# Optimization experiments

Hardware: AMD Instinct MI355X
Metric: run time of the kernel (lower is better)

Reference implementation:

```python
import jax, jax.numpy as jnp
import numpy as np

B, S, H, I, E, TOPK = 2, 2048, 1024, 2048, 8, 2


def setup_inputs() -> dict:
    key = jax.random.key(0)
    k0, k1, k2, k3, k4 = jax.random.split(key, 5)
    return {
        "hidden_state": jax.random.normal(k0, (B, S, H), dtype=jnp.float32),
        "gate_w": jax.random.normal(k1, (H, E), dtype=jnp.float32) * 0.02,
        "Wg": jax.random.normal(k2, (E, H, I), dtype=jnp.float32) * 0.02,
        "Wu": jax.random.normal(k3, (E, H, I), dtype=jnp.float32) * 0.02,
        "Wd": jax.random.normal(k4, (E, I, H), dtype=jnp.float32) * 0.02,
        "top_k": TOPK,
    }


def reference(hidden_state, gate_w, Wg, Wu, Wd, top_k):
    b, s, h = hidden_state.shape
    x = hidden_state.reshape(-1, h)                      # [T, H]
    T = x.shape[0]
    router_logits = x @ gate_w                           # [T, E]
    probs = jax.nn.softmax(router_logits, axis=-1)
    top_p, top_i = jax.lax.top_k(probs, top_k)           # [T, K]
    # norm_expert=False -> no renormalization of top-k probs
    # scatter top-k probs into dense per-expert combine weights [T, E]
    weights = jnp.zeros((T, probs.shape[-1]), dtype=x.dtype)
    weights = weights.at[jnp.arange(T)[:, None], top_i].add(top_p)
    # dense per-expert SwiGLU MLP (equivalent math to gather/scatter dispatch)
    g = jnp.einsum('th,ehi->tei', x, Wg)                 # [T, E, I]
    u = jnp.einsum('th,ehi->tei', x, Wu)
    mid = jax.nn.silu(g) * u
    expert_out = jnp.einsum('tei,eih->teh', mid, Wd)     # [T, E, H]
    final = jnp.einsum('te,teh->th', weights, expert_out)
    return final.reshape(b, s, h), router_logits
```

## Files before the change

kernel.cpp:

```cpp
#include <hip/hip_runtime.h>
#include <stdint.h>
#include <math.h>

#define T_TOK 4096
#define H_DIM 1024
#define I_DIM 2048
#define E_NUM 8
#define PMAX (T_TOK * 2 + E_NUM * 128)

typedef __attribute__((ext_vector_type(8))) short short8;
typedef __attribute__((ext_vector_type(4))) float f32x4;
typedef unsigned short u16;
typedef unsigned int u32;

__device__ __forceinline__ u16 f2bf(float f) {
  union { float f; u32 u; } v; v.f = f;
  u32 r = v.u + 0x7fffu + ((v.u >> 16) & 1u);
  return (u16)(r >> 16);
}
__device__ __forceinline__ float bf2f(u16 a) {
  union { u32 u; float f; } v; v.u = ((u32)a) << 16; return v.f;
}

__device__ __forceinline__ void async_ld16(const u16* g, u16* l) {
  __builtin_amdgcn_global_load_lds(
      (const __attribute__((address_space(1))) void*)g,
      (__attribute__((address_space(3))) void*)l, 16, 0, 0);
}

__global__ void prep_kernel(const float* __restrict__ x, u16* __restrict__ xb,
                            const float* __restrict__ gw, float* __restrict__ gwT, int n4) {
  int i = blockIdx.x * blockDim.x + threadIdx.x;
  int stride = gridDim.x * blockDim.x;
  for (int j = i; j < n4; j += stride) {
    float4 v = ((const float4*)x)[j];
    ushort4 o;
    o.x = f2bf(v.x); o.y = f2bf(v.y); o.z = f2bf(v.z); o.w = f2bf(v.w);
    ((ushort4*)xb)[j] = o;
  }
  if (i < H_DIM * E_NUM) {
    int r = i >> 3, e = i & 7;
    gwT[e * H_DIM + r] = gw[i];
  }
}

__global__ void wconv_kernel(const float* __restrict__ Wg, const float* __restrict__ Wu,
                             const float* __restrict__ Wd, u16* __restrict__ wgt,
                             u16* __restrict__ wut, u16* __restrict__ wdt) {
  const int zz = blockIdx.z;
  const float* src = (zz == 0) ? Wg : (zz == 1) ? Wu : Wd;
  u16* dst = (zz == 0) ? wgt : (zz == 1) ? wut : wdt;
  const int R = (zz == 2) ? I_DIM : H_DIM;
  const int C = (zz == 2) ? H_DIM : I_DIM;
  const int cpt = C >> 6;
  const int e = blockIdx.x >> 9;
  const int ti = blockIdx.x & 511;
  const int r0 = (ti / cpt) << 6;
  const int c0 = (ti % cpt) << 6;
  const float* s = src + (size_t)e * H_DIM * I_DIM;
  u16* d = dst + (size_t)e * H_DIM * I_DIM;

  const int wave = threadIdx.x >> 6, lane = threadIdx.x & 63;
  const int g = lane >> 4, lq = lane & 15;
  const int c = c0 + wave * 16 + g * 4;
  const int r = r0 + lq * 4;

  float4 v0 = *(const float4*)(s + (size_t)(r + 0) * C + c);
  float4 v1 = *(const float4*)(s + (size_t)(r + 1) * C + c);
  float4 v2 = *(const float4*)(s + (size_t)(r + 2) * C + c);
  float4 v3 = *(const float4*)(s + (size_t)(r + 3) * C + c);

  ushort4 o;
  o.x = f2bf(v0.x); o.y = f2bf(v1.x); o.z = f2bf(v2.x); o.w = f2bf(v3.x);
  *(ushort4*)(d + (size_t)(c + 0) * R + r) = o;
  o.x = f2bf(v0.y); o.y = f2bf(v1.y); o.z = f2bf(v2.y); o.w = f2bf(v3.y);
  *(ushort4*)(d + (size_t)(c + 1) * R + r) = o;
  o.x = f2bf(v0.z); o.y = f2bf(v1.z); o.z = f2bf(v2.z); o.w = f2bf(v3.z);
  *(ushort4*)(d + (size_t)(c + 2) * R + r) = o;
  o.x = f2bf(v0.w); o.y = f2bf(v1.w); o.z = f2bf(v2.w); o.w = f2bf(v3.w);
  *(ushort4*)(d + (size_t)(c + 3) * R + r) = o;
}

__global__ void router_kernel(const float* __restrict__ x, const float* __restrict__ gwT,
                              float* __restrict__ logits_out, int* __restrict__ te,
                              float* __restrict__ tw) {
  const int wave = threadIdx.x >> 6, lane = threadIdx.x & 63;
  const int t = blockIdx.x * 4 + wave;
  const float* xr = x + (size_t)t * H_DIM;
  float acc[8];
#pragma unroll
  for (int e = 0; e < 8; e++) acc[e] = 0.f;
#pragma unroll
  for (int it = 0; it < 4; it++) {
    int h0 = it * 256 + lane * 4;
    float4 xv = *(const float4*)(xr + h0);
#pragma unroll
    for (int e = 0; e < 8; e++) {
      float4 g = *(const float4*)(gwT + e * H_DIM + h0);
      acc[e] += xv.x * g.x + xv.y * g.y + xv.z * g.z + xv.w * g.w;
    }
  }
#pragma unroll
  for (int m = 1; m < 64; m <<= 1) {
#pragma unroll
    for (int e = 0; e < 8; e++) acc[e] += __shfl_xor(acc[e], m, 64);
  }
  if (lane == 0) {
    float mx = acc[0];
#pragma unroll
    for (int e = 1; e < 8; e++) mx = fmaxf(mx, acc[e]);
    float p[8]; float s = 0.f;
#pragma unroll
    for (int e = 0; e < 8; e++) { p[e] = __expf(acc[e] - mx); s += p[e]; }
    float inv = 1.0f / s;
    int e0 = 0; float b0 = acc[0];
#pragma unroll
    for (int e = 1; e < 8; e++) if (acc[e] > b0) { b0 = acc[e]; e0 = e; }
    int e1 = -1; float b1 = -1e30f;
#pragma unroll
    for (int e = 0; e < 8; e++) if (e != e0 && acc[e] > b1) { b1 = acc[e]; e1 = e; }
#pragma unroll
    for (int e = 0; e < 8; e++) logits_out[(size_t)t * 8 + e] = acc[e];
    te[t * 2] = e0; te[t * 2 + 1] = e1;
    tw[t * 2] = p[e0] * inv; tw[t * 2 + 1] = p[e1] * inv;
  }
}

__global__ __launch_bounds__(1024) void sort_kernel(const int* __restrict__ te,
                                                    int* __restrict__ offs,
                                                    int* __restrict__ token_list,
                                                    int* __restrict__ tpos) {
  __shared__ int wsum[16][8];
  __shared__ int wbase[16][8];
  __shared__ int soffs[9];
  const int tid = threadIdx.x;
  const int wave = tid >> 6, lane = tid & 63;

  for (int j = tid; j < PMAX; j += 1024) token_list[j] = 0;

  const int t0 = tid * 4;
  int e_loc[8];
  int cnt[8];
#pragma unroll
  for (int e = 0; e < 8; e++) cnt[e] = 0;
#pragma unroll
  for (int k = 0; k < 8; k++) {
    int e = te[t0 * 2 + k];
    e_loc[k] = e;
    cnt[e]++;
  }
  int excl[8];
#pragma unroll
  for (int e = 0; e < 8; e++) {
    int v = cnt[e];
    int s = v;
#pragma unroll
    for (int d = 1; d < 64; d <<= 1) {
      int u = __shfl_up(s, d, 64);
      if (lane >= d) s += u;
    }
    excl[e] = s - v;
    if (lane == 63) wsum[wave][e] = s;
  }
  __syncthreads();
  if (tid < 8) {
    int e = tid;
    int a = 0;
    for (int w2 = 0; w2 < 16; w2++) { wbase[w2][e] = a; a += wsum[w2][e]; }
    wsum[0][e] = a;
  }
  __syncthreads();
  if (tid == 0) {
    int a = 0;
    for (int e = 0; e < 8; e++) {
      soffs[e] = a;
      a += (wsum[0][e] + 127) & ~127;
    }
    soffs[8] = a;
    for (int e = 0; e <= 8; e++) offs[e] = soffs[e];
  }
  __syncthreads();
  int base[8];
#pragma unroll
  for (int e = 0; e < 8; e++) base[e] = soffs[e] + wbase[wave][e] + excl[e];
#pragma unroll
  for (int k = 0; k < 8; k++) {
    int e = e_loc[k];
    int pos = base[e]++;
    int t = t0 + (k >> 1);
    token_list[pos] = t;
    tpos[t * 2 + (k & 1)] = pos;
  }
}

#define BK1 64

__global__ __launch_bounds__(256, 2) void gemm1_kernel(
    const u16* __restrict__ xb, const u16* __restrict__ wgt, const u16* __restrict__ wut,
    const int* __restrict__ token_list, const int* __restrict__ offs, u16* __restrict__ mid) {
  const int e = blockIdx.z;
  const int off = offs[e];
  const int pcount = offs[e + 1] - off;
  const int row0 = blockIdx.y * 128;
  if (row0 >= pcount) return;
  const int n0 = blockIdx.x * 128;

  __shared__ __align__(16) u16 As[128 * BK1];
  __shared__ __align__(16) u16 Bg[128 * BK1];
  __shared__ __align__(16) u16 Bu[128 * BK1];

  const int tid = threadIdx.x;
  const int wave = tid >> 6, lane = tid & 63;
  const int wm = (wave >> 1) * 64, wn = (wave & 1) * 64;
  const int quad = lane >> 4, lr = lane & 15;
  const int l7 = lr & 7;

  f32x4 accg[4][4], accu[4][4];
  f32x4 z = {0.f, 0.f, 0.f, 0.f};
#pragma unroll
  for (int i = 0; i < 4; i++)
#pragma unroll
    for (int j = 0; j < 4; j++) { accg[i][j] = z; accu[i][j] = z; }

  const u16* wgb = wgt + (size_t)e * I_DIM * H_DIM;
  const u16* wub = wut + (size_t)e * I_DIM * H_DIM;

  const u16* ga[4]; const u16* gg[4]; const u16* gu[4];
  u16 *la[4], *lg[4], *lu[4];
#pragma unroll
  for (int i = 0; i < 4; i++) {
    int c = tid + 256 * i;
    int row = c >> 3, kcl = c & 7;
    int kg = kcl ^ (row & 7);
    int tok = token_list[off + row0 + row];
    ga[i] = xb + (size_t)tok * H_DIM + kg * 8;
    gg[i] = wgb + (size_t)(n0 + row) * H_DIM + kg * 8;
    gu[i] = wub + (size_t)(n0 + row) * H_DIM + kg * 8;
    la[i] = &As[c * 8]; lg[i] = &Bg[c * 8]; lu[i] = &Bu[c * 8];
  }

  for (int kt = 0; kt < H_DIM / BK1; kt++) {
    const int k0 = kt * BK1;
#pragma unroll
    for (int i = 0; i < 4; i++) {
      async_ld16(ga[i] + k0, la[i]);
      async_ld16(gg[i] + k0, lg[i]);
      async_ld16(gu[i] + k0, lu[i]);
    }
    __syncthreads();
#pragma unroll
    for (int kk = 0; kk < 2; kk++) {
      const int slot = ((kk << 2) + quad) ^ l7;
      short8 af[4];
#pragma unroll
      for (int im = 0; im < 4; im++)
        af[im] = *(const short8*)(&As[(wm + im * 16 + lr) * BK1 + slot * 8]);
#pragma unroll
      for (int in = 0; in < 4; in++) {
        short8 bg = *(const short8*)(&Bg[(wn + in * 16 + lr) * BK1 + slot * 8]);
        short8 bu = *(const short8*)(&Bu[(wn + in * 16 + lr) * BK1 + slot * 8]);
#pragma unroll
        for (int im = 0; im < 4; im++) {
          accg[im][in] = __builtin_amdgcn_mfma_f32_16x16x32_bf16(af[im], bg, accg[im][in], 0, 0, 0);
          accu[im][in] = __builtin_amdgcn_mfma_f32_16x16x32_bf16(af[im], bu, accu[im][in], 0, 0, 0);
        }
      }
    }
    __syncthreads();
  }

#pragma unroll
  for (int im = 0; im < 4; im++) {
#pragma unroll
    for (int r = 0; r < 4; r++) {
      int row = row0 + wm + im * 16 + quad * 4 + r;
      u16* mrow = mid + (size_t)(off + row) * I_DIM + n0 + wn;
#pragma unroll
      for (int in = 0; in < 4; in++) {
        float g = accg[im][in][r];
        float u = accu[im][in][r];
        float sv = g / (1.0f + __expf(-g)) * u;
        mrow[in * 16 + lr] = f2bf(sv);
      }
    }
  }
}

__global__ __launch_bounds__(256, 2) void gemm2_kernel(
    const u16* __restrict__ mid, const u16* __restrict__ wdt,
    const int* __restrict__ offs, u16* __restrict__ eout) {
  const int e = blockIdx.z;
  const int off = offs[e];
  const int pcount = offs[e + 1] - off;
  const int row0 = blockIdx.y * 128;
  if (row0 >= pcount) return;
  const int n0 = blockIdx.x * 128;

  __shared__ __align__(16) u16 As[128 * BK1];
  __shared__ __align__(16) u16 Bs[128 * BK1];

  const int tid = threadIdx.x;
  const int wave = tid >> 6, lane = tid & 63;
  const int wm = (wave >> 1) * 64, wn = (wave & 1) * 64;
  const int quad = lane >> 4, lr = lane & 15;
  const int l7 = lr & 7;

  f32x4 acc[4][4];
  f32x4 z = {0.f, 0.f, 0.f, 0.f};
#pragma unroll
  for (int i = 0; i < 4; i++)
#pragma unroll
    for (int j = 0; j < 4; j++) acc[i][j] = z;

  const u16* wdb = wdt + (size_t)e * H_DIM * I_DIM;

  const u16* ga[4]; const u16* gb[4];
  u16 *la[4], *lb[4];
#pragma unroll
  for (int i = 0; i < 4; i++) {
    int c = tid + 256 * i;
    int row = c >> 3, kcl = c & 7;
    int kg = kcl ^ (row & 7);
    ga[i] = mid + (size_t)(off + row0 + row) * I_DIM + kg * 8;
    gb[i] = wdb + (size_t)(n0 + row) * I_DIM + kg * 8;
    la[i] = &As[c * 8]; lb[i] = &Bs[c * 8];
  }

  for (int kt = 0; kt < I_DIM / BK1; kt++) {
    const int k0 = kt * BK1;
#pragma unroll
    for (int i = 0; i < 4; i++) {
      async_ld16(ga[i] + k0, la[i]);
      async_ld16(gb[i] + k0, lb[i]);
    }
    __syncthreads();
#pragma unroll
    for (int kk = 0; kk < 2; kk++) {
      const int slot = ((kk << 2) + quad) ^ l7;
      short8 af[4];
#pragma unroll
      for (int im = 0; im < 4; im++)
        af[im] = *(const short8*)(&As[(wm + im * 16 + lr) * BK1 + slot * 8]);
#pragma unroll
      for (int in = 0; in < 4; in++) {
        short8 bf = *(const short8*)(&Bs[(wn + in * 16 + lr) * BK1 + slot * 8]);
#pragma unroll
        for (int im = 0; im < 4; im++)
          acc[im][in] = __builtin_amdgcn_mfma_f32_16x16x32_bf16(af[im], bf, acc[im][in], 0, 0, 0);
      }
    }
    __syncthreads();
  }

#pragma unroll
  for (int im = 0; im < 4; im++) {
#pragma unroll
    for (int r = 0; r < 4; r++) {
      int row = row0 + wm + im * 16 + quad * 4 + r;
      u16* orow = eout + (size_t)(off + row) * H_DIM + n0 + wn;
#pragma unroll
      for (int in = 0; in < 4; in++)
        orow[in * 16 + lr] = f2bf(acc[im][in][r]);
    }
  }
}

__global__ void combine_kernel(const u16* __restrict__ eout, const int* __restrict__ tpos,
                               const float* __restrict__ tw, float* __restrict__ out) {
  const int half = threadIdx.x >> 7;
  const int t = blockIdx.x * 2 + half;
  const int lt = threadIdx.x & 127;
  const int h0 = lt * 8;
  const int p0 = tpos[t * 2], p1 = tpos[t * 2 + 1];
  const float w0 = tw[t * 2], w1 = tw[t * 2 + 1];
  ushort4 a0 = *(const ushort4*)(eout + (size_t)p0 * H_DIM + h0);
  ushort4 a1 = *(const ushort4*)(eout + (size_t)p0 * H_DIM + h0 + 4);
  ushort4 b0 = *(const ushort4*)(eout + (size_t)p1 * H_DIM + h0);
  ushort4 b1 = *(const ushort4*)(eout + (size_t)p1 * H_DIM + h0 + 4);
  float4 o0, o1;
  o0.x = w0 * bf2f(a0.x) + w1 * bf2f(b0.x);
  o0.y = w0 * bf2f(a0.y) + w1 * bf2f(b0.y);
  o0.z = w0 * bf2f(a0.z) + w1 * bf2f(b0.z);
  o0.w = w0 * bf2f(a0.w) + w1 * bf2f(b0.w);
  o1.x = w0 * bf2f(a1.x) + w1 * bf2f(b1.x);
  o1.y = w0 * bf2f(a1.y) + w1 * bf2f(b1.y);
  o1.z = w0 * bf2f(a1.z) + w1 * bf2f(b1.z);
  o1.w = w0 * bf2f(a1.w) + w1 * bf2f(b1.w);
  float* orow = out + (size_t)t * H_DIM + h0;
  *(float4*)(orow) = o0;
  *(float4*)(orow + 4) = o1;
}

extern "C" void kernel_launch(void* const* d_in, const int* in_sizes, int n_in,
                              void* d_out, int out_size, void* d_ws, size_t ws_size,
                              hipStream_t stream) {
  const float* x  = (const float*)d_in[0];
  const float* gw = (const float*)d_in[1];
  const float* Wg = (const float*)d_in[2];
  const float* Wu = (const float*)d_in[3];
  const float* Wd = (const float*)d_in[4];
  float* out = (float*)d_out;
  float* out_logits = out + (size_t)T_TOK * H_DIM;

  char* w = (char*)d_ws;
  size_t o = 0;
  auto take = [&](size_t bytes) { char* p = w + o; o += (bytes + 255) & ~(size_t)255; return p; };
  int*   offs        = (int*)take((E_NUM + 1) * 4);
  int*   te          = (int*)take((size_t)T_TOK * 2 * 4);
  float* tw          = (float*)take((size_t)T_TOK * 2 * 4);
  int*   token_list  = (int*)take((size_t)PMAX * 4);
  int*   tpos        = (int*)take((size_t)T_TOK * 2 * 4);
  float* gwT         = (float*)take((size_t)E_NUM * H_DIM * 4);
  u16*   xb          = (u16*)take((size_t)T_TOK * H_DIM * 2);
  u16*   wgt         = (u16*)take((size_t)E_NUM * H_DIM * I_DIM * 2);
  u16*   wut         = (u16*)take((size_t)E_NUM * H_DIM * I_DIM * 2);
  u16*   wdt         = (u16*)take((size_t)E_NUM * H_DIM * I_DIM * 2);
  u16*   mid         = (u16*)take((size_t)PMAX * I_DIM * 2);
  u16*   eout        = wgt;
  (void)in_sizes; (void)n_in; (void)out_size; (void)ws_size;

  prep_kernel<<<512, 256, 0, stream>>>(x, xb, gw, gwT, T_TOK * H_DIM / 4);
  wconv_kernel<<<dim3(E_NUM * 512, 1, 3), 256, 0, stream>>>(Wg, Wu, Wd, wgt, wut, wdt);
  router_kernel<<<T_TOK / 4, 256, 0, stream>>>(x, gwT, out_logits, te, tw);
  sort_kernel<<<1, 1024, 0, stream>>>(te, offs, token_list, tpos);
  gemm1_kernel<<<dim3(I_DIM / 128, PMAX / 128, E_NUM), 256, 0, stream>>>(xb, wgt, wut, token_list, offs, mid);
  gemm2_kernel<<<dim3(H_DIM / 128, PMAX / 128, E_NUM), 256, 0, stream>>>(mid, wdt, offs, eout);
  combine_kernel<<<T_TOK / 2, 256, 0, stream>>>(eout, tpos, tw, out);
}
```

Measured before the change: 420.1 us.

## Fuse weight conversion, x cast and router into one front kernel; raise GEMM occupancy hints

Merges the weight bf16 transpose, activation bf16 cast and router into a single launch. Router blocks stage the transposed gate weights in shared memory, which removes the separate gwT buffer and pass. Launch bounds on the two grouped GEMMs are raised to request more resident blocks per CU. Risks are register spills in the GEMMs and the 32KB static LDS lowering occupancy of the weight-conversion blocks.

```diff
diff --git a/kernel.cpp b/kernel.cpp
--- a/kernel.cpp
+++ b/kernel.cpp
@@ -8,6 +8,9 @@
 #define E_NUM 8
 #define PMAX (T_TOK * 2 + E_NUM * 128)
 
+#define WCONV_BLOCKS (E_NUM * 512 * 3)
+#define ROUTER_BLOCKS (T_TOK / 4)
+
 typedef __attribute__((ext_vector_type(8))) short short8;
 typedef __attribute__((ext_vector_type(4))) float f32x4;
 typedef unsigned short u16;
@@ -28,101 +31,103 @@
       (__attribute__((address_space(3))) void*)l, 16, 0, 0);
 }
 
-__global__ void prep_kernel(const float* __restrict__ x, u16* __restrict__ xb,
-                            const float* __restrict__ gw, float* __restrict__ gwT, int n4) {
-  int i = blockIdx.x * blockDim.x + threadIdx.x;
-  int stride = gridDim.x * blockDim.x;
-  for (int j = i; j < n4; j += stride) {
-    float4 v = ((const float4*)x)[j];
+__global__ void front_kernel(const float* __restrict__ Wg, const float* __restrict__ Wu,
+                             const float* __restrict__ Wd, u16* __restrict__ wgt,
+                             u16* __restrict__ wut, u16* __restrict__ wdt,
+                             const float* __restrict__ x, u16* __restrict__ xb,
+                             const float* __restrict__ gw, float* __restrict__ logits_out,
+                             int* __restrict__ te, float* __restrict__ tw) {
+  __shared__ float sgw[E_NUM * H_DIM];
+  const int b = blockIdx.x;
+  if (b < WCONV_BLOCKS) {
+    const int zz = b / (E_NUM * 512);
+    const int idx = b - zz * (E_NUM * 512);
+    const float* src = (zz == 0) ? Wg : (zz == 1) ? Wu : Wd;
+    u16* dst = (zz == 0) ? wgt : (zz == 1) ? wut : wdt;
+    const int R = (zz == 2) ? I_DIM : H_DIM;
+    const int C = (zz == 2) ? H_DIM : I_DIM;
+    const int cpt = C >> 6;
+    const int e = idx >> 9;
+    const int ti = idx & 511;
+    const int r0 = (ti / cpt) << 6;
+    const int c0 = (ti % cpt) << 6;
+    const float* s = src + (size_t)e * H_DIM * I_DIM;
+    u16* d = dst + (size_t)e * H_DIM * I_DIM;
+
+    const int wave = threadIdx.x >> 6, lane = threadIdx.x & 63;
+    const int g = lane >> 4, lq = lane & 15;
+    const int c = c0 + wave * 16 + g * 4;
+    const int r = r0 + lq * 4;
+
+    float4 v0 = *(const float4*)(s + (size_t)(r + 0) * C + c);
+    float4 v1 = *(const float4*)(s + (size_t)(r + 1) * C + c);
+    float4 v2 = *(const float4*)(s + (size_t)(r + 2) * C + c);
+    float4 v3 = *(const float4*)(s + (size_t)(r + 3) * C + c);
+
     ushort4 o;
-    o.x = f2bf(v.x); o.y = f2bf(v.y); o.z = f2bf(v.z); o.w = f2bf(v.w);
-    ((ushort4*)xb)[j] = o;
-  }
-  if (i < H_DIM * E_NUM) {
-    int r = i >> 3, e = i & 7;
-    gwT[e * H_DIM + r] = gw[i];
-  }
-}
-
-__global__ void wconv_kernel(const float* __restrict__ Wg, const float* __restrict__ Wu,
-                             const float* __restrict__ Wd, u16* __restrict__ wgt,
-                             u16* __restrict__ wut, u16* __restrict__ wdt) {
-  const int zz = blockIdx.z;
-  const float* src = (zz == 0) ? Wg : (zz == 1) ? Wu : Wd;
-  u16* dst = (zz == 0) ? wgt : (zz == 1) ? wut : wdt;
-  const int R = (zz == 2) ? I_DIM : H_DIM;
-  const int C = (zz == 2) ? H_DIM : I_DIM;
-  const int cpt = C >> 6;
-  const int e = blockIdx.x >> 9;
-  const int ti = blockIdx.x & 511;
-  const int r0 = (ti / cpt) << 6;
-  const int c0 = (ti % cpt) << 6;
-  const float* s = src + (size_t)e * H_DIM * I_DIM;
-  u16* d = dst + (size_t)e * H_DIM * I_DIM;
-
-  const int wave = threadIdx.x >> 6, lane = threadIdx.x & 63;
-  const int g = lane >> 4, lq = lane & 15;
-  const int c = c0 + wave * 16 + g * 4;
-  const int r = r0 + lq * 4;
-
-  float4 v0 = *(const float4*)(s + (size_t)(r + 0) * C + c);
-  float4 v1 = *(const float4*)(s + (size_t)(r + 1) * C + c);
-  float4 v2 = *(const float4*)(s + (size_t)(r + 2) * C + c);
-  float4 v3 = *(const float4*)(s + (size_t)(r + 3) * C + c);
-
-  ushort4 o;
-  o.x = f2bf(v0.x); o.y = f2bf(v1.x); o.z = f2bf(v2.x); o.w = f2bf(v3.x);
-  *(ushort4*)(d + (size_t)(c + 0) * R + r) = o;
-  o.x = f2bf(v0.y); o.y = f2bf(v1.y); o.z = f2bf(v2.y); o.w = f2bf(v3.y);
-  *(ushort4*)(d + (size_t)(c + 1) * R + r) = o;
-  o.x = f2bf(v0.z); o.y = f2bf(v1.z); o.z = f2bf(v2.z); o.w = f2bf(v3.z);
-  *(ushort4*)(d + (size_t)(c + 2) * R + r) = o;
-  o.x = f2bf(v0.w); o.y = f2bf(v1.w); o.z = f2bf(v2.w); o.w = f2bf(v3.w);
-  *(ushort4*)(d + (size_t)(c + 3) * R + r) = o;
-}
-
-__global__ void router_kernel(const float* __restrict__ x, const float* __restrict__ gwT,
-                              float* __restrict__ logits_out, int* __restrict__ te,
-                              float* __restrict__ tw) {
-  const int wave = threadIdx.x >> 6, lane = threadIdx.x & 63;
-  const int t = blockIdx.x * 4 + wave;
-  const float* xr = x + (size_t)t * H_DIM;
-  float acc[8];
-#pragma unroll
-  for (int e = 0; e < 8; e++) acc[e] = 0.f;
-#pragma unroll
-  for (int it = 0; it < 4; it++) {
-    int h0 = it * 256 + lane * 4;
-    float4 xv = *(const float4*)(xr + h0);
-#pragma unroll
-    for (int e = 0; e < 8; e++) {
-      float4 g = *(const float4*)(gwT + e * H_DIM + h0);
-      acc[e] += xv.x * g.x + xv.y * g.y + xv.z * g.z + xv.w * g.w;
-    }
-  }
-#pragma unroll
-  for (int m = 1; m < 64; m <<= 1) {
-#pragma unroll
-    for (int e = 0; e < 8; e++) acc[e] += __shfl_xor(acc[e], m, 64);
-  }
-  if (lane == 0) {
-    float mx = acc[0];
-#pragma unroll
-    for (int e = 1; e < 8; e++) mx = fmaxf(mx, acc[e]);
-    float p[8]; float s = 0.f;
-#pragma unroll
-    for (int e = 0; e < 8; e++) { p[e] = __expf(acc[e] - mx); s += p[e]; }
-    float inv = 1.0f / s;
-    int e0 = 0; float b0 = acc[0];
-#pragma unroll
-    for (int e = 1; e < 8; e++) if (acc[e] > b0) { b0 = acc[e]; e0 = e; }
-    int e1 = -1; float b1 = -1e30f;
-#pragma unroll
-    for (int e = 0; e < 8; e++) if (e != e0 && acc[e] > b1) { b1 = acc[e]; e1 = e; }
-#pragma unroll
-    for (int e = 0; e < 8; e++) logits_out[(size_t)t * 8 + e] = acc[e];
-    te[t * 2] = e0; te[t * 2 + 1] = e1;
-    tw[t * 2] = p[e0] * inv; tw[t * 2 + 1] = p[e1] * inv;
+    o.x = f2bf(v0.x); o.y = f2bf(v1.x); o.z = f2bf(v2.x); o.w = f2bf(v3.x);
+    *(ushort4*)(d + (size_t)(c + 0) * R + r) = o;
+    o.x = f2bf(v0.y); o.y = f2bf(v1.y); o.z = f2bf(v2.y); o.w = f2bf(v3.y);
+    *(ushort4*)(d + (size_t)(c + 1) * R + r) = o;
+    o.x = f2bf(v0.z); o.y = f2bf(v1.z); o.z = f2bf(v2.z); o.w = f2bf(v3.z);
+    *(ushort4*)(d + (size_t)(c + 2) * R + r) = o;
+    o.x = f2bf(v0.w); o.y = f2bf(v1.w); o.z = f2bf(v2.w); o.w = f2bf(v3.w);
+    *(ushort4*)(d + (size_t)(c + 3) * R + r) = o;
+  } else {
+    const int rb = b - WCONV_BLOCKS;
+    for (int j = threadIdx.x; j < (H_DIM * E_NUM) / 4; j += 256) {
+      float4 v = ((const float4*)gw)[j];
+      int base = j * 4;
+      sgw[((base + 0) & 7) * H_DIM + ((base + 0) >> 3)] = v.x;
+      sgw[((base + 1) & 7) * H_DIM + ((base + 1) >> 3)] = v.y;
+      sgw[((base + 2) & 7) * H_DIM + ((base + 2) >> 3)] = v.z;
+      sgw[((base + 3) & 7) * H_DIM + ((base + 3) >> 3)] = v.w;
+    }
+    __syncthreads();
+    const int wave = threadIdx.x >> 6, lane = threadIdx.x & 63;
+    const int t = rb * 4 + wave;
+    const float* xr = x + (size_t)t * H_DIM;
+    u16* xbr = xb + (size_t)t * H_DIM;
+    float acc[8];
+#pragma unroll
+    for (int e = 0; e < 8; e++) acc[e] = 0.f;
+#pragma unroll
+    for (int it = 0; it < 4; it++) {
+      int h0 = it * 256 + lane * 4;
+      float4 xv = *(const float4*)(xr + h0);
+      ushort4 o;
+      o.x = f2bf(xv.x); o.y = f2bf(xv.y); o.z = f2bf(xv.z); o.w = f2bf(xv.w);
+      *(ushort4*)(xbr + h0) = o;
+#pragma unroll
+      for (int e = 0; e < 8; e++) {
+        float4 g = *(const float4*)(&sgw[e * H_DIM + h0]);
+        acc[e] += xv.x * g.x + xv.y * g.y + xv.z * g.z + xv.w * g.w;
+      }
+    }
+#pragma unroll
+    for (int m = 1; m < 64; m <<= 1) {
+#pragma unroll
+      for (int e = 0; e < 8; e++) acc[e] += __shfl_xor(acc[e], m, 64);
+    }
+    if (lane == 0) {
+      float mx = acc[0];
+#pragma unroll
+      for (int e = 1; e < 8; e++) mx = fmaxf(mx, acc[e]);
+      float p[8]; float s = 0.f;
+#pragma unroll
+      for (int e = 0; e < 8; e++) { p[e] = __expf(acc[e] - mx); s += p[e]; }
+      float inv = 1.0f / s;
+      int e0 = 0; float b0 = acc[0];
+#pragma unroll
+      for (int e = 1; e < 8; e++) if (acc[e] > b0) { b0 = acc[e]; e0 = e; }
+      int e1 = -1; float b1 = -1e30f;
+#pragma unroll
+      for (int e = 0; e < 8; e++) if (e != e0 && acc[e] > b1) { b1 = acc[e]; e1 = e; }
+#pragma unroll
+      for (int e = 0; e < 8; e++) logits_out[(size_t)t * 8 + e] = acc[e];
+      te[t * 2] = e0; te[t * 2 + 1] = e1;
+      tw[t * 2] = p[e0] * inv; tw[t * 2 + 1] = p[e1] * inv;
+    }
   }
 }
 
@@ -195,7 +200,7 @@
 
 #define BK1 64
 
-__global__ __launch_bounds__(256, 2) void gemm1_kernel(
+__global__ __launch_bounds__(256, 3) void gemm1_kernel(
     const u16* __restrict__ xb, const u16* __restrict__ wgt, const u16* __restrict__ wut,
     const int* __restrict__ token_list, const int* __restrict__ offs, u16* __restrict__ mid) {
   const int e = blockIdx.z;
@@ -286,7 +291,7 @@
   }
 }
 
-__global__ __launch_bounds__(256, 2) void gemm2_kernel(
+__global__ __launch_bounds__(256, 4) void gemm2_kernel(
     const u16* __restrict__ mid, const u16* __restrict__ wdt,
     const int* __restrict__ offs, u16* __restrict__ eout) {
   const int e = blockIdx.z;
@@ -410,7 +415,6 @@
   float* tw          = (float*)take((size_t)T_TOK * 2 * 4);
   int*   token_list  = (int*)take((size_t)PMAX * 4);
   int*   tpos        = (int*)take((size_t)T_TOK * 2 * 4);
-  float* gwT         = (float*)take((size_t)E_NUM * H_DIM * 4);
   u16*   xb          = (u16*)take((size_t)T_TOK * H_DIM * 2);
   u16*   wgt         = (u16*)take((size_t)E_NUM * H_DIM * I_DIM * 2);
   u16*   wut         = (u16*)take((size_t)E_NUM * H_DIM * I_DIM * 2);
@@ -419,9 +423,8 @@
   u16*   eout        = wgt;
   (void)in_sizes; (void)n_in; (void)out_size; (void)ws_size;
 
-  prep_kernel<<<512, 256, 0, stream>>>(x, xb, gw, gwT, T_TOK * H_DIM / 4);
-  wconv_kernel<<<dim3(E_NUM * 512, 1, 3), 256, 0, stream>>>(Wg, Wu, Wd, wgt, wut, wdt);
-  router_kernel<<<T_TOK / 4, 256, 0, stream>>>(x, gwT, out_logits, te, tw);
+  front_kernel<<<WCONV_BLOCKS + ROUTER_BLOCKS, 256, 0, stream>>>(
+      Wg, Wu, Wd, wgt, wut, wdt, x, xb, gw, out_logits, te, tw);
   sort_kernel<<<1, 1024, 0, stream>>>(te, offs, token_list, tpos);
   gemm1_kernel<<<dim3(I_DIM / 128, PMAX / 128, E_NUM), 256, 0, stream>>>(xb, wgt, wut, token_list, offs, mid);
   gemm2_kernel<<<dim3(H_DIM / 128, PMAX / 128, E_NUM), 256, 0, stream>>>(mid, wdt, offs, eout);
```

Result: slower. 482.1 us (+14.8%).
